# Optimization experiments

Measured on AMD Instinct MI355X. Metric: run time of the kernel, lower is better.

The kernel has to match this reference:

```python
import jax, jax.numpy as jnp
import numpy as np

HEAD_SIZE = 64
N_EMBED = 1024

def setup_inputs() -> dict:
    key = jax.random.key(0)
    kx, kk, kq, kv = jax.random.split(key, 4)
    x = jax.random.normal(kx, (8, 2048, N_EMBED), dtype=jnp.float32)
    # torch nn.Linear weights: [out_features, in_features]
    s = 1.0 / np.sqrt(N_EMBED)
    Wk = jax.random.uniform(kk, (HEAD_SIZE, N_EMBED), jnp.float32, -s, s)
    Wq = jax.random.uniform(kq, (HEAD_SIZE, N_EMBED), jnp.float32, -s, s)
    Wv = jax.random.uniform(kv, (HEAD_SIZE, N_EMBED), jnp.float32, -s, s)
    return {"x": x, "Wk": Wk, "Wq": Wq, "Wv": Wv}

def reference(x, Wk, Wq, Wv):
    B, T, C = x.shape
    k = x @ Wk.T  # [B,T,H]
    q = x @ Wq.T
    v = x @ Wv.T
    # NOTE: original computes k @ q^T and scales by sqrt(C)=sqrt(n_embed)
    wei = jnp.einsum('btd,bsd->bts', k, q) / jnp.sqrt(jnp.float32(C))
    mask = jnp.tril(jnp.ones((T, T), dtype=bool))
    wei = jnp.where(mask, wei, -jnp.inf)
    wei = jax.nn.softmax(wei, axis=-1)
    return wei @ v  # [B,T,H]
```

## Files before the change

### kernel.cpp

```cpp
#include <hip/hip_runtime.h>
#include <hip/hip_bf16.h>


typedef __attribute__((ext_vector_type(8))) short short8;
typedef __attribute__((ext_vector_type(4))) float f32x4;
typedef __attribute__((ext_vector_type(16))) float f32x16;
typedef __attribute__((ext_vector_type(2))) unsigned int u32x2;
typedef unsigned int u32;

#define BATCH 8
#define T 2048
#define CDIM 1024
#define HD 64
#define QK_SCALE 0.04508422f

static __device__ __forceinline__ short f2bf(float f) {
    return __builtin_bit_cast(short, __float2bfloat16(f));
}
static __device__ __forceinline__ float bf2f(unsigned short s) {
    u32 u = ((u32)s) << 16;
    return __builtin_bit_cast(float, u);
}
static __device__ __forceinline__ u32 packbf(float lo, float hi) {
    return (u32)(unsigned short)f2bf(lo) | ((u32)(unsigned short)f2bf(hi) << 16);
}
static __device__ __forceinline__ f32x4 mfma16(short8 a, short8 b, f32x4 c) {
    return __builtin_amdgcn_mfma_f32_16x16x32_bf16(a, b, c, 0, 0, 0);
}
static __device__ __forceinline__ f32x16 mfma32(short8 a, short8 b, f32x16 c) {
    return __builtin_amdgcn_mfma_f32_32x32x16_bf16(a, b, c, 0, 0, 0);
}

__global__ __launch_bounds__(256) void wcvt_kernel(
    const float* __restrict__ Wk, const float* __restrict__ Wq,
    const float* __restrict__ Wv, short* __restrict__ wfrag)
{
    const int t = blockIdx.x * 256 + threadIdx.x;
    const int lane = t & 63, kk = (t >> 6) & 31, d16 = (t >> 11) & 3, p = t >> 13;
    const float* __restrict__ W = (p == 0) ? Wk : (p == 1 ? Wq : Wv);
    const float sc = (p == 0) ? QK_SCALE : 1.0f;
    const float* src = W + (size_t)(d16 * 16 + (lane & 15)) * CDIM
                         + kk * 32 + ((lane >> 4) & 3) * 8;
    f32x4 a = *(const f32x4*)src;
    f32x4 b = *(const f32x4*)(src + 4);
    short8 o;
#pragma unroll
    for (int e = 0; e < 4; ++e) { o[e] = f2bf(a[e] * sc); o[e + 4] = f2bf(b[e] * sc); }
    *(short8*)(wfrag + (size_t)t * 8) = o;
}

#define PLOAD(KC) \
    _Pragma("unroll") for (int u = 0; u < 8; ++u) \
        xr[u] = *(const f32x4*)(x + (size_t)(row0 + u * 8 + wid) * CDIM + (KC) * 256 + lane * 4);

#define PWRITE(BUF) \
    _Pragma("unroll") for (int u = 0; u < 8; ++u) { \
        u32x2 pk2 = { packbf(xr[u][0], xr[u][1]), packbf(xr[u][2], xr[u][3]) }; \
        *(u32x2*)&xs[BUF][(u * 8 + wid) * 512 + ((lane * 8) ^ ((wid & 7) << 4))] = pk2; }

#define PCOMPUTE(KC, BUF) \
    _Pragma("unroll") for (int kk = 0; kk < 8; ++kk) { \
        short8 af0 = *(short8*)&xs[BUF][(rg * 32 + c) * 512 + ((kk * 64 + g * 16) ^ ((c & 7) << 4))]; \
        short8 af1 = *(short8*)&xs[BUF][(rg * 32 + 16 + c) * 512 + ((kk * 64 + g * 16) ^ ((c & 7) << 4))]; \
        _Pragma("unroll") for (int j = 0; j < 3; ++j) { \
            short8 bf = *(const short8*)&wfrag[(size_t)((cg * 3 + j) * 32 + (KC) * 8 + kk) * 512 + lane * 8]; \
            acc[0][j] = mfma16(af0, bf, acc[0][j]); \
            acc[1][j] = mfma16(af1, bf, acc[1][j]); } }

__global__ __launch_bounds__(512, 2) void proj_kernel(
    const float* __restrict__ x, const short* __restrict__ wfrag,
    short* __restrict__ kfrag, short* __restrict__ qfrag, short* __restrict__ vfrag)
{
    __shared__ __align__(16) char xs[2][32768];

    const int tid = threadIdx.x, wid = tid >> 6, lane = tid & 63;
    const int c = lane & 15, g = lane >> 4;
    const int l5 = lane & 31, h = lane >> 5;
    const int row0 = blockIdx.x * 64;
    const int rg = wid >> 2, cg = wid & 3;

    f32x4 xr[8];
    f32x4 acc[2][3] = {};

    PLOAD(0)
    PWRITE(0)
    __syncthreads();

    PLOAD(1)
    PCOMPUTE(0, 0)
    PWRITE(1)
    __syncthreads();

    PLOAD(2)
    PCOMPUTE(1, 1)
    PWRITE(0)
    __syncthreads();

    PLOAD(3)
    PCOMPUTE(2, 0)
    PWRITE(1)
    __syncthreads();

    PCOMPUTE(3, 1)
    __syncthreads();

    short* st_k = (short*)&xs[0][0];
    short* st_q = (short*)&xs[0][9216];
    short* st_v = (short*)&xs[0][18432];
#pragma unroll
    for (int j = 0; j < 3; ++j) {
        const int q = cg * 3 + j, p = q >> 2, d16 = q & 3;
#pragma unroll
        for (int rh = 0; rh < 2; ++rh)
#pragma unroll
            for (int r = 0; r < 4; ++r) {
                const int mrow = rg * 32 + rh * 16 + g * 4 + r;
                const short v = f2bf(acc[rh][j][r]);
                if (p == 0)      st_k[mrow * 72 + d16 * 16 + c] = v;
                else if (p == 1) st_q[mrow * 72 + d16 * 16 + c] = v;
                else             st_v[(d16 * 16 + c) * 72 + mrow] = v;
            }
    }
    __syncthreads();

    const int bb = row0 >> 11, ti0 = (row0 & 2047) >> 5;
    const int th = wid >> 2, fq = wid & 3;
    const size_t tbase = ((size_t)(bb * 64 + ti0 + th)) * 4 + fq;

    short8 kv = *(short8*)&st_k[(th * 32 + l5) * 72 + fq * 16 + h * 8];
    *(short8*)&kfrag[tbase * 512 + lane * 8] = kv;
    short8 qv = *(short8*)&st_q[(th * 32 + l5) * 72 + fq * 16 + h * 8];
    *(short8*)&qfrag[tbase * 512 + lane * 8] = qv;
    const int dh = fq >> 1, ssub = fq & 1;
    short8 vv = *(short8*)&st_v[(dh * 32 + l5) * 72 + th * 32 + ssub * 16 + h * 8];
    *(short8*)&vfrag[tbase * 512 + lane * 8] = vv;
}

__global__ __launch_bounds__(512) void attn_kernel(
    const short* __restrict__ kfrag, const short* __restrict__ qfrag,
    const short* __restrict__ vfrag, float* __restrict__ out)
{
    const int tid = threadIdx.x, wid = tid >> 6, lane = tid & 63;
    const int l5 = lane & 31, h = lane >> 5;
    const int bx = blockIdx.x;
    const int i = 63 - (bx >> 3);
    const int b = bx & 7;
    const int t0 = i * 32;

    __shared__ u32   sO[8][32][32];
    __shared__ float sML[8][2][32];

    const short* __restrict__ kb = kfrag + ((size_t)(b * 64 + i)) * 2048;
    const short* __restrict__ qb = qfrag + ((size_t)b * 64) * 2048;
    const short* __restrict__ vb = vfrag + ((size_t)b * 64) * 2048;

    short8 kf[4];
#pragma unroll
    for (int ks = 0; ks < 4; ++ks)
        kf[ks] = *(const short8*)&kb[ks * 512 + lane * 8];

    float m = -1e30f, l = 0.f;
    f32x16 o0 = {}, o1 = {};

    short8 qf[4], vf[4], qn[4], vn[4];
#pragma unroll
    for (int ks = 0; ks < 4; ++ks) {
        qf[ks] = *(const short8*)&qb[((size_t)wid * 4 + ks) * 512 + lane * 8];
        vf[ks] = *(const short8*)&vb[((size_t)wid * 4 + ks) * 512 + lane * 8];
    }

    for (int st = wid; st <= i; st += 8) {
        f32x16 Cs = {};
#pragma unroll
        for (int ks = 0; ks < 4; ++ks)
            Cs = mfma32(qf[ks], kf[ks], Cs);

        if (st + 8 <= i) {
#pragma unroll
            for (int ks = 0; ks < 4; ++ks) {
                qn[ks] = *(const short8*)&qb[((size_t)(st + 8) * 4 + ks) * 512 + lane * 8];
                vn[ks] = *(const short8*)&vb[((size_t)(st + 8) * 4 + ks) * 512 + lane * 8];
            }
        }

        if (st == i) {
#pragma unroll
            for (int r = 0; r < 16; ++r) {
                const int srow = (r & 3) + 8 * (r >> 2) + 4 * h;
                if (srow > l5) Cs[r] = -1e30f;
            }
        }
        float mx = fmaxf(Cs[0], Cs[1]);
#pragma unroll
        for (int r = 2; r < 16; ++r) mx = fmaxf(mx, Cs[r]);
        mx = fmaxf(mx, __shfl_xor(mx, 32));
        if (!__all(mx <= m)) {
            const float mnew = fmaxf(m, mx);
            const float alpha = exp2f(m - mnew);
            m = mnew;
            l *= alpha;
#pragma unroll
            for (int r = 0; r < 16; ++r) { o0[r] *= alpha; o1[r] *= alpha; }
        }
        u32 pk[8];
        float rs = 0.f;
#pragma unroll
        for (int q = 0; q < 8; ++q) {
            const float e0 = exp2f(Cs[2 * q] - m);
            const float e1 = exp2f(Cs[2 * q + 1] - m);
            rs += e0 + e1;
            pk[q] = packbf(e0, e1);
        }
        rs += __shfl_xor(rs, 32);
        l += rs;

        u32 w0 = pk[0], w2 = pk[2];
        asm volatile("v_permlane32_swap_b32 %0, %1" : "+v"(w0), "+v"(w2));
        u32 w1 = pk[1], w3 = pk[3];
        asm volatile("v_permlane32_swap_b32 %0, %1" : "+v"(w1), "+v"(w3));
        u32 w4 = pk[4], w6 = pk[6];
        asm volatile("v_permlane32_swap_b32 %0, %1" : "+v"(w4), "+v"(w6));
        u32 w5 = pk[5], w7 = pk[7];
        asm volatile("v_permlane32_swap_b32 %0, %1" : "+v"(w5), "+v"(w7));
        short8 pf0, pf1;
        pf0[0] = (short)(w0 & 0xffff); pf0[1] = (short)(w0 >> 16);
        pf0[2] = (short)(w1 & 0xffff); pf0[3] = (short)(w1 >> 16);
        pf0[4] = (short)(w2 & 0xffff); pf0[5] = (short)(w2 >> 16);
        pf0[6] = (short)(w3 & 0xffff); pf0[7] = (short)(w3 >> 16);
        pf1[0] = (short)(w4 & 0xffff); pf1[1] = (short)(w4 >> 16);
        pf1[2] = (short)(w5 & 0xffff); pf1[3] = (short)(w5 >> 16);
        pf1[4] = (short)(w6 & 0xffff); pf1[5] = (short)(w6 >> 16);
        pf1[6] = (short)(w7 & 0xffff); pf1[7] = (short)(w7 >> 16);

        o0 = mfma32(vf[0], pf0, o0);
        o0 = mfma32(vf[1], pf1, o0);
        o1 = mfma32(vf[2], pf0, o1);
        o1 = mfma32(vf[3], pf1, o1);

#pragma unroll
        for (int ks = 0; ks < 4; ++ks) { qf[ks] = qn[ks]; vf[ks] = vn[ks]; }
    }

#pragma unroll
    for (int q = 0; q < 8; ++q) {
        const int dp = (q & 1) + 4 * (q >> 1) + 2 * h;
        sO[wid][dp][l5]      = packbf(o0[2 * q], o0[2 * q + 1]);
        sO[wid][16 + dp][l5] = packbf(o1[2 * q], o1[2 * q + 1]);
    }
    if (h == 0) { sML[wid][0][l5] = m; sML[wid][1][l5] = l; }
    __syncthreads();

    float M = -1e30f;
#pragma unroll
    for (int p = 0; p < 8; ++p) M = fmaxf(M, sML[p][0][l5]);
    float L = 0.f;
    float av[4] = {};
#pragma unroll
    for (int p = 0; p < 8; ++p) {
        const float w = exp2f(sML[p][0][l5] - M);
        L += w * sML[p][1][l5];
#pragma unroll
        for (int dd2 = 0; dd2 < 2; ++dd2) {
            const u32 v = sO[p][wid * 4 + h * 2 + dd2][l5];
            av[2 * dd2]     += w * bf2f((unsigned short)(v & 0xffff));
            av[2 * dd2 + 1] += w * bf2f((unsigned short)(v >> 16));
        }
    }
    const float inv = 1.f / L;
    f32x4 r = { av[0] * inv, av[1] * inv, av[2] * inv, av[3] * inv };
    *(f32x4*)&out[((size_t)b * T + t0 + l5) * HD + wid * 8 + h * 4] = r;
}

extern "C" void kernel_launch(void* const* d_in, const int* in_sizes, int n_in,
                              void* d_out, int out_size, void* d_ws, size_t ws_size,
                              hipStream_t stream) {
    const float* x  = (const float*)d_in[0];
    const float* Wk = (const float*)d_in[1];
    const float* Wq = (const float*)d_in[2];
    const float* Wv = (const float*)d_in[3];
    float* out = (float*)d_out;

    short* kfrag = (short*)d_ws;
    short* qfrag = kfrag + (size_t)BATCH * T * HD;
    short* vfrag = qfrag + (size_t)BATCH * T * HD;
    short* wfrag = vfrag + (size_t)BATCH * T * HD;

    wcvt_kernel<<<96, 256, 0, stream>>>(Wk, Wq, Wv, wfrag);
    proj_kernel<<<256, 512, 0, stream>>>(x, wfrag, kfrag, qfrag, vfrag);
    attn_kernel<<<512, 512, 0, stream>>>(kfrag, qfrag, vfrag, out);
}
```

Measured before the change: 49.42 us.

## Shrink projection tiles to 16 rows and load x directly into registers

The projection kernel moves from 64-row tiles with 512 threads, double-buffered LDS staging of x and a two-row-group split, to 16-row tiles with 256 threads. Each wave now reads x straight from global memory into MFMA A-fragments, with no LDS staging. The grid grows from 256 to 1024 blocks to spread the memory-bound x read across more CUs. In exchange, each weight fragment is reloaded by four times as many blocks, and global x reads are strided per lane rather than coalesced row reads.

```diff
diff --git a/kernel.cpp b/kernel.cpp
--- a/kernel.cpp
+++ b/kernel.cpp
@@ -5,7 +5,6 @@
 typedef __attribute__((ext_vector_type(8))) short short8;
 typedef __attribute__((ext_vector_type(4))) float f32x4;
 typedef __attribute__((ext_vector_type(16))) float f32x16;
-typedef __attribute__((ext_vector_type(2))) unsigned int u32x2;
 typedef unsigned int u32;
 
 #define BATCH 8
@@ -49,91 +48,66 @@
     *(short8*)(wfrag + (size_t)t * 8) = o;
 }
 
-#define PLOAD(KC) \
-    _Pragma("unroll") for (int u = 0; u < 8; ++u) \
-        xr[u] = *(const f32x4*)(x + (size_t)(row0 + u * 8 + wid) * CDIM + (KC) * 256 + lane * 4);
-
-#define PWRITE(BUF) \
-    _Pragma("unroll") for (int u = 0; u < 8; ++u) { \
-        u32x2 pk2 = { packbf(xr[u][0], xr[u][1]), packbf(xr[u][2], xr[u][3]) }; \
-        *(u32x2*)&xs[BUF][(u * 8 + wid) * 512 + ((lane * 8) ^ ((wid & 7) << 4))] = pk2; }
-
-#define PCOMPUTE(KC, BUF) \
-    _Pragma("unroll") for (int kk = 0; kk < 8; ++kk) { \
-        short8 af0 = *(short8*)&xs[BUF][(rg * 32 + c) * 512 + ((kk * 64 + g * 16) ^ ((c & 7) << 4))]; \
-        short8 af1 = *(short8*)&xs[BUF][(rg * 32 + 16 + c) * 512 + ((kk * 64 + g * 16) ^ ((c & 7) << 4))]; \
-        _Pragma("unroll") for (int j = 0; j < 3; ++j) { \
-            short8 bf = *(const short8*)&wfrag[(size_t)((cg * 3 + j) * 32 + (KC) * 8 + kk) * 512 + lane * 8]; \
-            acc[0][j] = mfma16(af0, bf, acc[0][j]); \
-            acc[1][j] = mfma16(af1, bf, acc[1][j]); } }
-
-__global__ __launch_bounds__(512, 2) void proj_kernel(
+__global__ __launch_bounds__(256) void proj_kernel(
     const float* __restrict__ x, const short* __restrict__ wfrag,
     short* __restrict__ kfrag, short* __restrict__ qfrag, short* __restrict__ vfrag)
 {
-    __shared__ __align__(16) char xs[2][32768];
-
-    const int tid = threadIdx.x, wid = tid >> 6, lane = tid & 63;
+    __shared__ __align__(16) short st_k[16 * 72];
+    __shared__ __align__(16) short st_q[16 * 72];
+    __shared__ __align__(16) short st_v[64 * 24];
+
+    const int tid = threadIdx.x, cg = tid >> 6, lane = tid & 63;
     const int c = lane & 15, g = lane >> 4;
-    const int l5 = lane & 31, h = lane >> 5;
-    const int row0 = blockIdx.x * 64;
-    const int rg = wid >> 2, cg = wid & 3;
-
-    f32x4 xr[8];
-    f32x4 acc[2][3] = {};
-
-    PLOAD(0)
-    PWRITE(0)
-    __syncthreads();
-
-    PLOAD(1)
-    PCOMPUTE(0, 0)
-    PWRITE(1)
-    __syncthreads();
-
-    PLOAD(2)
-    PCOMPUTE(1, 1)
-    PWRITE(0)
-    __syncthreads();
-
-    PLOAD(3)
-    PCOMPUTE(2, 0)
-    PWRITE(1)
-    __syncthreads();
-
-    PCOMPUTE(3, 1)
-    __syncthreads();
-
-    short* st_k = (short*)&xs[0][0];
-    short* st_q = (short*)&xs[0][9216];
-    short* st_v = (short*)&xs[0][18432];
+    const int row0 = blockIdx.x * 16;
+    const float* __restrict__ xr = x + (size_t)(row0 + c) * CDIM + g * 8;
+
+    f32x4 acc[3] = {};
+#pragma unroll 4
+    for (int kk = 0; kk < 32; ++kk) {
+        const float* ax = xr + kk * 32;
+        f32x4 a0 = *(const f32x4*)ax;
+        f32x4 a1 = *(const f32x4*)(ax + 4);
+        short8 af = { f2bf(a0[0]), f2bf(a0[1]), f2bf(a0[2]), f2bf(a0[3]),
+                      f2bf(a1[0]), f2bf(a1[1]), f2bf(a1[2]), f2bf(a1[3]) };
+#pragma unroll
+        for (int j = 0; j < 3; ++j) {
+            const int q = cg * 3 + j;
+            short8 bf = *(const short8*)&wfrag[(size_t)(q * 32 + kk) * 512 + lane * 8];
+            acc[j] = mfma16(af, bf, acc[j]);
+        }
+    }
+
 #pragma unroll
     for (int j = 0; j < 3; ++j) {
         const int q = cg * 3 + j, p = q >> 2, d16 = q & 3;
 #pragma unroll
-        for (int rh = 0; rh < 2; ++rh)
-#pragma unroll
-            for (int r = 0; r < 4; ++r) {
-                const int mrow = rg * 32 + rh * 16 + g * 4 + r;
-                const short v = f2bf(acc[rh][j][r]);
-                if (p == 0)      st_k[mrow * 72 + d16 * 16 + c] = v;
-                else if (p == 1) st_q[mrow * 72 + d16 * 16 + c] = v;
-                else             st_v[(d16 * 16 + c) * 72 + mrow] = v;
-            }
+        for (int r = 0; r < 4; ++r) {
+            const int row = g * 4 + r;
+            const short v = f2bf(acc[j][r]);
+            if (p == 0)      st_k[row * 72 + d16 * 16 + c] = v;
+            else if (p == 1) st_q[row * 72 + d16 * 16 + c] = v;
+            else             st_v[(d16 * 16 + c) * 24 + row] = v;
+        }
     }
     __syncthreads();
 
-    const int bb = row0 >> 11, ti0 = (row0 & 2047) >> 5;
-    const int th = wid >> 2, fq = wid & 3;
-    const size_t tbase = ((size_t)(bb * 64 + ti0 + th)) * 4 + fq;
-
-    short8 kv = *(short8*)&st_k[(th * 32 + l5) * 72 + fq * 16 + h * 8];
-    *(short8*)&kfrag[tbase * 512 + lane * 8] = kv;
-    short8 qv = *(short8*)&st_q[(th * 32 + l5) * 72 + fq * 16 + h * 8];
-    *(short8*)&qfrag[tbase * 512 + lane * 8] = qv;
-    const int dh = fq >> 1, ssub = fq & 1;
-    short8 vv = *(short8*)&st_v[(dh * 32 + l5) * 72 + th * 32 + ssub * 16 + h * 8];
-    *(short8*)&vfrag[tbase * 512 + lane * 8] = vv;
+    const int b = row0 >> 11, i = (row0 & 2047) >> 5, ssub = (row0 >> 4) & 1;
+    const size_t tb = ((size_t)(b * 64 + i)) * 4;
+    const int l5 = lane & 31, h = lane >> 5;
+    const int ks = cg;
+
+    if ((l5 >> 4) == ssub) {
+        const int rl = l5 & 15;
+        short8 kv = *(short8*)&st_k[rl * 72 + ks * 16 + h * 8];
+        *(short8*)&kfrag[(tb + ks) * 512 + lane * 8] = kv;
+        short8 qv = *(short8*)&st_q[rl * 72 + ks * 16 + h * 8];
+        *(short8*)&qfrag[(tb + ks) * 512 + lane * 8] = qv;
+    }
+    if (cg < 2) {
+        const int dh = cg;
+        short8 vv = *(short8*)&st_v[(dh * 32 + l5) * 24 + h * 8];
+        *(short8*)&vfrag[(tb + dh * 2 + ssub) * 512 + lane * 8] = vv;
+    }
 }
 
 __global__ __launch_bounds__(512) void attn_kernel(
@@ -286,6 +260,6 @@
     short* wfrag = vfrag + (size_t)BATCH * T * HD;
 
     wcvt_kernel<<<96, 256, 0, stream>>>(Wk, Wq, Wv, wfrag);
-    proj_kernel<<<256, 512, 0, stream>>>(x, wfrag, kfrag, qfrag, vfrag);
+    proj_kernel<<<1024, 256, 0, stream>>>(x, wfrag, kfrag, qfrag, vfrag);
     attn_kernel<<<512, 512, 0, stream>>>(kfrag, qfrag, vfrag, out);
 }
```

Result: slower. 79.48 us (+60.8%).
